# Kernel tuning notes

Hardware: AMD Instinct MI355X
Metric: run time of the kernel (lower is better)

Reference implementation:

```python
import jax, jax.numpy as jnp
import numpy as np

KERNEL = (3, 3, 3)
STRIDE = (1, 1, 1)
PAD = (1, 1, 1)
DIL = (1, 1, 1)


def _deform_unfold_3d(x, offset):
    # x: [B, C, D, H, W]; offset: [B, 3*K, Do, Ho, Wo] with per-tap (dd, dh, dw) order.
    B, C, D, H, W = x.shape
    kd, kh, kw = KERNEL
    K = kd * kh * kw
    Do = (D + 2 * PAD[0] - (DIL[0] * (kd - 1) + 1)) // STRIDE[0] + 1
    Ho = (H + 2 * PAD[1] - (DIL[1] * (kh - 1) + 1)) // STRIDE[1] + 1
    Wo = (W + 2 * PAD[2] - (DIL[2] * (kw - 1) + 1)) // STRIDE[2] + 1
    P = Do * Ho * Wo
    dt = x.dtype
    # kernel-tap base displacements, flattened to [K]
    ki, kj, kk = jnp.meshgrid(jnp.arange(kd), jnp.arange(kh), jnp.arange(kw), indexing="ij")
    bd = (ki.reshape(-1) * DIL[0] - PAD[0]).astype(dt)
    bh = (kj.reshape(-1) * DIL[1] - PAD[1]).astype(dt)
    bw = (kk.reshape(-1) * DIL[2] - PAD[2]).astype(dt)
    # output-grid anchor positions, flattened to [P]
    od, oh, ow = jnp.meshgrid(jnp.arange(Do), jnp.arange(Ho), jnp.arange(Wo), indexing="ij")
    gd = (od.reshape(-1) * STRIDE[0]).astype(dt)
    gh = (oh.reshape(-1) * STRIDE[1]).astype(dt)
    gw = (ow.reshape(-1) * STRIDE[2]).astype(dt)
    off = offset.reshape(B, K, 3, P)
    # sampling positions [B, K, P]
    pd = bd[None, :, None] + gd[None, None, :] + off[:, :, 0]
    ph = bh[None, :, None] + gh[None, None, :] + off[:, :, 1]
    pw = bw[None, :, None] + gw[None, None, :] + off[:, :, 2]
    d0f = jnp.floor(pd); fd = pd - d0f; d0 = d0f.astype(jnp.int32)
    h0f = jnp.floor(ph); fh = ph - h0f; h0 = h0f.astype(jnp.int32)
    w0f = jnp.floor(pw); fw = pw - w0f; w0 = w0f.astype(jnp.int32)
    xflat = x.reshape(B, C, D * H * W)
    out = jnp.zeros((B, C, K, P), dt)
    for ci in (0, 1):
        dsel = d0 + ci
        wd = (1.0 - fd) if ci == 0 else fd
        for cj in (0, 1):
            hsel = h0 + cj
            wh = (1.0 - fh) if cj == 0 else fh
            for ck in (0, 1):
                wsel = w0 + ck
                ww = (1.0 - fw) if ck == 0 else fw
                valid = (dsel >= 0) & (dsel < D) & (hsel >= 0) & (hsel < H) & (wsel >= 0) & (wsel < W)
                idx = (jnp.clip(dsel, 0, D - 1) * H + jnp.clip(hsel, 0, H - 1)) * W + jnp.clip(wsel, 0, W - 1)
                wgt = jnp.where(valid, wd * wh * ww, jnp.zeros((), dt))  # [B, K, P]
                val = jnp.take_along_axis(xflat, idx.reshape(B, 1, K * P), axis=2).reshape(B, C, K, P)
                out = out + wgt[:, None] * val
    return out.reshape(B, C * K, P)  # im2col columns, channel-major then kernel tap


def setup_inputs() -> dict:
    key = jax.random.key(0)
    k1, k2 = jax.random.split(key)
    inp = jax.random.normal(k1, (2, 16, 24, 48, 48), dtype=jnp.float32)
    offset = jax.random.normal(k2, (2, 81, 24, 48, 48), dtype=jnp.float32)
    return {"input": inp, "offset": offset}


def reference(input, offset):
    return _deform_unfold_3d(input, offset)
```

## Files before the change

### kernel.cpp

```cpp
#include <hip/hip_runtime.h>
#include <hip/hip_bf16.h>

typedef float f4 __attribute__((ext_vector_type(4)));
typedef unsigned int u32;
typedef u32 u4 __attribute__((ext_vector_type(4)));

constexpr int B = 2, C = 16, D = 24, H = 48, W = 48;
constexpr int K = 27;
constexpr int SP = D * H * W;
constexpr int HW = H * W;

__device__ inline ushort bf16_bits(float f) {
    __hip_bfloat16 h = __float2bfloat16(f);
    return __builtin_bit_cast(ushort, h);
}

__global__ __launch_bounds__(256) void xpose_bf16_kernel(const float* __restrict__ x,
                                                         u32* __restrict__ xt) {
    int t = blockIdx.x * blockDim.x + threadIdx.x;
    if (t >= B * SP) return;
    int s = t % SP, b = t / SP;
    const float* src = x + (size_t)b * C * SP + s;
    u4 pk[2];
#pragma unroll
    for (int m = 0; m < 8; ++m) {
        float lo = src[(size_t)(2 * m) * SP];
        float hi = src[(size_t)(2 * m + 1) * SP];
        pk[m >> 2][m & 3] = (u32)bf16_bits(lo) | ((u32)bf16_bits(hi) << 16);
    }
    u4* dst = reinterpret_cast<u4*>(xt + (size_t)t * 8);
    dst[0] = pk[0];
    dst[1] = pk[1];
}

__global__ __launch_bounds__(256, 8) void deform_bf16_kernel(const u32* __restrict__ xt,
                                                             const float* __restrict__ off,
                                                             float* __restrict__ out) {
    const int tid = blockIdx.x * blockDim.x + threadIdx.x;
    const int q = tid & 1;
    const int u = tid >> 1;
    const int p = u % SP;
    const int bk = u / SP;
    const int k = bk % K, b = bk / K;

    const float* ob = off + ((size_t)b * (3 * K) + 3 * k) * SP + p;
    float offd = __builtin_nontemporal_load(ob);
    float offh = __builtin_nontemporal_load(ob + (size_t)SP);
    float offw = __builtin_nontemporal_load(ob + (size_t)2 * SP);

    int od = p / HW, rem = p - od * HW;
    int oh = rem / W, ow = rem - oh * W;
    int ki = k / 9, kr = k - ki * 9;
    int kj = kr / 3, kk = kr - kj * 3;

    float pd = (float)(od + ki - 1) + offd;
    float ph = (float)(oh + kj - 1) + offh;
    float pw = (float)(ow + kk - 1) + offw;

    float d0f = floorf(pd), h0f = floorf(ph), w0f = floorf(pw);
    float fd = pd - d0f, fh = ph - h0f, fw = pw - w0f;
    int d0 = (int)d0f, h0 = (int)h0f, w0 = (int)w0f;

    const u4* xb = reinterpret_cast<const u4*>(xt) + (size_t)b * SP * 2 + q;

    float acc[8] = {};
#pragma unroll
    for (int ci = 0; ci < 2; ++ci) {
        int ds = d0 + ci;
        bool vd = (ds >= 0) & (ds < D);
        float wd = ci ? fd : 1.0f - fd;
        int dc = min(max(ds, 0), D - 1);
#pragma unroll
        for (int cj = 0; cj < 2; ++cj) {
            int hs = h0 + cj;
            bool vh = (hs >= 0) & (hs < H);
            float wh = cj ? fh : 1.0f - fh;
            int hc = min(max(hs, 0), H - 1);
#pragma unroll
            for (int ck = 0; ck < 2; ++ck) {
                int ws = w0 + ck;
                bool vw = (ws >= 0) & (ws < W);
                float ww = ck ? fw : 1.0f - fw;
                int wc = min(max(ws, 0), W - 1);
                float wgt = (vd & vh & vw) ? wd * wh * ww : 0.0f;
                int idx = (dc * H + hc) * W + wc;
                u4 v = xb[(size_t)idx * 2];
#pragma unroll
                for (int m = 0; m < 4; ++m) {
                    u32 wbits = v[m];
                    float lo = __builtin_bit_cast(float, wbits << 16);
                    float hi = __builtin_bit_cast(float, wbits & 0xffff0000u);
                    acc[2 * m] += wgt * lo;
                    acc[2 * m + 1] += wgt * hi;
                }
            }
        }
    }

    __shared__ float lds[4][16][36];
    const int l = threadIdx.x & 63;
    const int wv = threadIdx.x >> 6;
    const int c = l >> 1;
    float(*tile)[36] = lds[wv];
#pragma unroll
    for (int j = 0; j < 8; ++j) tile[8 * q + j][c] = acc[j];
    __syncthreads();

    const size_t p_base = (size_t)(p - c);
    float* obase = out + (((size_t)b * C) * K + k) * SP + p_base;
#pragma unroll
    for (int r = 0; r < 2; ++r) {
        int ch = 8 * r + (l >> 3);
        int p0 = 4 * (l & 7);
        f4 v = *reinterpret_cast<const f4*>(&tile[ch][p0]);
        *reinterpret_cast<f4*>(obase + (size_t)ch * K * SP + p0) = v;
    }
}

__global__ __launch_bounds__(256) void deform_kernel_nat(const float* __restrict__ x,
                                                         const float* __restrict__ off,
                                                         float* __restrict__ out) {
    int tid = blockIdx.x * blockDim.x + threadIdx.x;
    if (tid >= B * K * SP) return;
    int p = tid % SP;
    int bk = tid / SP;
    int k = bk % K, b = bk / K;

    const float* ob = off + ((size_t)b * (3 * K) + 3 * k) * SP + p;
    float offd = ob[0];
    float offh = ob[(size_t)SP];
    float offw = ob[(size_t)2 * SP];

    int od = p / HW, rem = p - od * HW;
    int oh = rem / W, ow = rem - oh * W;
    int ki = k / 9, kr = k - ki * 9;
    int kj = kr / 3, kk = kr - kj * 3;

    float pd = (float)(od + ki - 1) + offd;
    float ph = (float)(oh + kj - 1) + offh;
    float pw = (float)(ow + kk - 1) + offw;

    float d0f = floorf(pd), h0f = floorf(ph), w0f = floorf(pw);
    float fd = pd - d0f, fh = ph - h0f, fw = pw - w0f;
    int d0 = (int)d0f, h0 = (int)h0f, w0 = (int)w0f;

    f4 acc[4] = {};
#pragma unroll
    for (int ci = 0; ci < 2; ++ci) {
        int ds = d0 + ci;
        bool vd = (ds >= 0) & (ds < D);
        float wd = ci ? fd : 1.0f - fd;
        int dc = min(max(ds, 0), D - 1);
#pragma unroll
        for (int cj = 0; cj < 2; ++cj) {
            int hs = h0 + cj;
            bool vh = (hs >= 0) & (hs < H);
            float wh = cj ? fh : 1.0f - fh;
            int hc = min(max(hs, 0), H - 1);
#pragma unroll
            for (int ck = 0; ck < 2; ++ck) {
                int ws = w0 + ck;
                bool vw = (ws >= 0) & (ws < W);
                float ww = ck ? fw : 1.0f - fw;
                int wc = min(max(ws, 0), W - 1);
                float wgt = (vd & vh & vw) ? wd * wh * ww : 0.0f;
                int idx = (dc * H + hc) * W + wc;
                const float* src = x + (size_t)b * C * SP + idx;
#pragma unroll
                for (int c2 = 0; c2 < C; ++c2)
                    acc[c2 >> 2][c2 & 3] += wgt * src[(size_t)c2 * SP];
            }
        }
    }

    float* o = out + ((size_t)b * C * K + k) * SP + p;
#pragma unroll
    for (int c2 = 0; c2 < C; ++c2)
        o[(size_t)c2 * K * SP] = acc[c2 >> 2][c2 & 3];
}

extern "C" void kernel_launch(void* const* d_in, const int* in_sizes, int n_in,
                              void* d_out, int out_size, void* d_ws, size_t ws_size,
                              hipStream_t stream) {
    const float* x = (const float*)d_in[0];
    const float* off = (const float*)d_in[1];
    float* out = (float*)d_out;

    const size_t xt_bytes = (size_t)B * SP * 16 * sizeof(ushort);

    if (ws_size >= xt_bytes) {
        u32* xt = (u32*)d_ws;
        const int n_x = B * SP;
        xpose_bf16_kernel<<<(n_x + 255) / 256, 256, 0, stream>>>(x, xt);
        const long long n2 = (long long)B * K * SP * 2;
        const int grid2 = (int)((n2 + 255) / 256);
        deform_bf16_kernel<<<grid2, 256, 0, stream>>>(xt, off, out);
    } else {
        const int n_main = B * K * SP;
        deform_kernel_nat<<<(n_main + 255) / 256, 256, 0, stream>>>(x, off, out);
    }
}
```

Before: 116.3 us.

## Loop each thread over half the kernel taps with double-buffered LDS tiles

The deformable gather kernel now gives each thread a fixed (batch, position, channel-half) and has it loop over 13 or 14 kernel taps, instead of launching one thread per tap. The LDS transpose tile is double-buffered by tap parity, so each iteration needs one barrier before the coalesced output store. This cuts per-thread index setup and launch size, and may improve locality of gathers across neighbouring taps. In exchange the grid shrinks by roughly a factor of 13, which lowers occupancy and leaves less parallelism to hide gather latency.

```diff
diff --git a/kernel.cpp b/kernel.cpp
--- a/kernel.cpp
+++ b/kernel.cpp
@@ -33,87 +33,96 @@
     dst[1] = pk[1];
 }
 
-__global__ __launch_bounds__(256, 8) void deform_bf16_kernel(const u32* __restrict__ xt,
-                                                             const float* __restrict__ off,
-                                                             float* __restrict__ out) {
+__global__ __launch_bounds__(256, 8) void deform_bf16_k(const u32* __restrict__ xt,
+                                                        const float* __restrict__ off,
+                                                        float* __restrict__ out) {
     const int tid = blockIdx.x * blockDim.x + threadIdx.x;
     const int q = tid & 1;
-    const int u = tid >> 1;
-    const int p = u % SP;
-    const int bk = u / SP;
-    const int k = bk % K, b = bk / K;
-
-    const float* ob = off + ((size_t)b * (3 * K) + 3 * k) * SP + p;
-    float offd = __builtin_nontemporal_load(ob);
-    float offh = __builtin_nontemporal_load(ob + (size_t)SP);
-    float offw = __builtin_nontemporal_load(ob + (size_t)2 * SP);
-
-    int od = p / HW, rem = p - od * HW;
-    int oh = rem / W, ow = rem - oh * W;
-    int ki = k / 9, kr = k - ki * 9;
-    int kj = kr / 3, kk = kr - kj * 3;
-
-    float pd = (float)(od + ki - 1) + offd;
-    float ph = (float)(oh + kj - 1) + offh;
-    float pw = (float)(ow + kk - 1) + offw;
-
-    float d0f = floorf(pd), h0f = floorf(ph), w0f = floorf(pw);
-    float fd = pd - d0f, fh = ph - h0f, fw = pw - w0f;
-    int d0 = (int)d0f, h0 = (int)h0f, w0 = (int)w0f;
-
+    const int t = tid >> 1;
+    const int p = t % SP;
+    const int r = t / SP;
+    const int khalf = r & 1;
+    const int b = r >> 1;
+
+    const int od = p / HW;
+    const int rem = p - od * HW;
+    const int oh = rem / W, ow = rem - oh * W;
+
+    const float* obp = off + (size_t)b * (3 * K) * SP + p;
     const u4* xb = reinterpret_cast<const u4*>(xt) + (size_t)b * SP * 2 + q;
 
-    float acc[8] = {};
-#pragma unroll
-    for (int ci = 0; ci < 2; ++ci) {
-        int ds = d0 + ci;
-        bool vd = (ds >= 0) & (ds < D);
-        float wd = ci ? fd : 1.0f - fd;
-        int dc = min(max(ds, 0), D - 1);
-#pragma unroll
-        for (int cj = 0; cj < 2; ++cj) {
-            int hs = h0 + cj;
-            bool vh = (hs >= 0) & (hs < H);
-            float wh = cj ? fh : 1.0f - fh;
-            int hc = min(max(hs, 0), H - 1);
-#pragma unroll
-            for (int ck = 0; ck < 2; ++ck) {
-                int ws = w0 + ck;
-                bool vw = (ws >= 0) & (ws < W);
-                float ww = ck ? fw : 1.0f - fw;
-                int wc = min(max(ws, 0), W - 1);
-                float wgt = (vd & vh & vw) ? wd * wh * ww : 0.0f;
-                int idx = (dc * H + hc) * W + wc;
-                u4 v = xb[(size_t)idx * 2];
-#pragma unroll
-                for (int m = 0; m < 4; ++m) {
-                    u32 wbits = v[m];
-                    float lo = __builtin_bit_cast(float, wbits << 16);
-                    float hi = __builtin_bit_cast(float, wbits & 0xffff0000u);
-                    acc[2 * m] += wgt * lo;
-                    acc[2 * m + 1] += wgt * hi;
+    __shared__ float lds[2][4][16][36];
+    const int l = threadIdx.x & 63;
+    const int wv = threadIdx.x >> 6;
+    const int c = l >> 1;
+    const size_t p_base = (size_t)(p - c);
+    const int ch_lo = l >> 3;
+    const int p0 = 4 * (l & 7);
+    float* osb = out + ((size_t)b * C * K) * SP + p_base + p0;
+
+    const int k_beg = khalf ? 14 : 0;
+    const int k_end = khalf ? 27 : 14;
+#pragma unroll 2
+    for (int k = k_beg; k < k_end; ++k) {
+        const int ki = k / 9, kr2 = k - ki * 9;
+        const int kj = kr2 / 3, kk = kr2 - kj * 3;
+
+        float offd = __builtin_nontemporal_load(obp + (size_t)(3 * k) * SP);
+        float offh = __builtin_nontemporal_load(obp + (size_t)(3 * k + 1) * SP);
+        float offw = __builtin_nontemporal_load(obp + (size_t)(3 * k + 2) * SP);
+
+        float pd = (float)(od + ki - 1) + offd;
+        float ph = (float)(oh + kj - 1) + offh;
+        float pw = (float)(ow + kk - 1) + offw;
+
+        float d0f = floorf(pd), h0f = floorf(ph), w0f = floorf(pw);
+        float fd = pd - d0f, fh = ph - h0f, fw = pw - w0f;
+        int d0 = (int)d0f, h0 = (int)h0f, w0 = (int)w0f;
+
+        float acc[8] = {};
+#pragma unroll
+        for (int ci = 0; ci < 2; ++ci) {
+            int ds = d0 + ci;
+            bool vd = (ds >= 0) & (ds < D);
+            float wd = ci ? fd : 1.0f - fd;
+            int dc = min(max(ds, 0), D - 1);
+#pragma unroll
+            for (int cj = 0; cj < 2; ++cj) {
+                int hs = h0 + cj;
+                bool vh = (hs >= 0) & (hs < H);
+                float wh = cj ? fh : 1.0f - fh;
+                int hc = min(max(hs, 0), H - 1);
+#pragma unroll
+                for (int ck = 0; ck < 2; ++ck) {
+                    int ws = w0 + ck;
+                    bool vw = (ws >= 0) & (ws < W);
+                    float ww = ck ? fw : 1.0f - fw;
+                    int wc = min(max(ws, 0), W - 1);
+                    float wgt = (vd & vh & vw) ? wd * wh * ww : 0.0f;
+                    int idx = (dc * H + hc) * W + wc;
+                    u4 v = xb[(size_t)idx * 2];
+#pragma unroll
+                    for (int m = 0; m < 4; ++m) {
+                        u32 wbits = v[m];
+                        float lo = __builtin_bit_cast(float, wbits << 16);
+                        float hi = __builtin_bit_cast(float, wbits & 0xffff0000u);
+                        acc[2 * m] += wgt * lo;
+                        acc[2 * m + 1] += wgt * hi;
+                    }
                 }
             }
         }
-    }
-
-    __shared__ float lds[4][16][36];
-    const int l = threadIdx.x & 63;
-    const int wv = threadIdx.x >> 6;
-    const int c = l >> 1;
-    float(*tile)[36] = lds[wv];
-#pragma unroll
-    for (int j = 0; j < 8; ++j) tile[8 * q + j][c] = acc[j];
-    __syncthreads();
-
-    const size_t p_base = (size_t)(p - c);
-    float* obase = out + (((size_t)b * C) * K + k) * SP + p_base;
-#pragma unroll
-    for (int r = 0; r < 2; ++r) {
-        int ch = 8 * r + (l >> 3);
-        int p0 = 4 * (l & 7);
-        f4 v = *reinterpret_cast<const f4*>(&tile[ch][p0]);
-        *reinterpret_cast<f4*>(obase + (size_t)ch * K * SP + p0) = v;
+
+        float(*tile)[36] = lds[k & 1][wv];
+#pragma unroll
+        for (int j = 0; j < 8; ++j) tile[8 * q + j][c] = acc[j];
+        __syncthreads();
+#pragma unroll
+        for (int rr = 0; rr < 2; ++rr) {
+            int ch = 8 * rr + ch_lo;
+            f4 vv = *reinterpret_cast<const f4*>(&tile[ch][p0]);
+            *reinterpret_cast<f4*>(osb + ((size_t)ch * K + k) * SP) = vv;
+        }
     }
 }
 
@@ -192,9 +201,9 @@
         u32* xt = (u32*)d_ws;
         const int n_x = B * SP;
         xpose_bf16_kernel<<<(n_x + 255) / 256, 256, 0, stream>>>(x, xt);
-        const long long n2 = (long long)B * K * SP * 2;
-        const int grid2 = (int)((n2 + 255) / 256);
-        deform_bf16_kernel<<<grid2, 256, 0, stream>>>(xt, off, out);
+        const long long n_thr = (long long)B * SP * 2 * 2;
+        const int grid = (int)(n_thr / 256);
+        deform_bf16_k<<<grid, 256, 0, stream>>>(xt, off, out);
     } else {
         const int n_main = B * K * SP;
         deform_kernel_nat<<<(n_main + 255) / 256, 256, 0, stream>>>(x, off, out);
```

Result: slower. 146.5 us (+26.0%).

## Compute all 16 channels per thread instead of splitting across thread pairs

Applied to the files above, without the earlier changes.

Each thread now handles one (b,k,p) sample with all 16 channels, loading both 16-byte bf16 records per corner, instead of two threads splitting 8 channels each. This halves the thread count and removes the duplicated offset loads, index math and bilinear weight computation per sample. The LDS transpose tile grows to 64 positions per wave and stores go out as 256-byte contiguous rows per channel. Per-thread register use rises, and the launch bound drops to 4 blocks per CU, which may reduce occupancy and memory-latency hiding for the gathers.

```diff
diff --git a/kernel.cpp b/kernel.cpp
--- a/kernel.cpp
+++ b/kernel.cpp
@@ -33,26 +33,25 @@
     dst[1] = pk[1];
 }
 
-__global__ __launch_bounds__(256, 8) void deform_bf16_kernel(const u32* __restrict__ xt,
-                                                             const float* __restrict__ off,
-                                                             float* __restrict__ out) {
+__global__ __launch_bounds__(256, 4) void deform_bf16_c16(const u32* __restrict__ xt,
+                                                          const float* __restrict__ off,
+                                                          float* __restrict__ out) {
     const int tid = blockIdx.x * blockDim.x + threadIdx.x;
-    const int q = tid & 1;
-    const int u = tid >> 1;
-    const int p = u % SP;
-    const int bk = u / SP;
+    const int p = tid % SP;
+    const int bk = tid / SP;
     const int k = bk % K, b = bk / K;
+
+    const int od = p / HW;
+    const int rem = p - od * HW;
+    const int oh = rem / W, ow = rem - oh * W;
+    const int ki = k / 9, kr2 = k - ki * 9;
+    const int kj = kr2 / 3, kk = kr2 - kj * 3;
 
     const float* ob = off + ((size_t)b * (3 * K) + 3 * k) * SP + p;
     float offd = __builtin_nontemporal_load(ob);
     float offh = __builtin_nontemporal_load(ob + (size_t)SP);
     float offw = __builtin_nontemporal_load(ob + (size_t)2 * SP);
 
-    int od = p / HW, rem = p - od * HW;
-    int oh = rem / W, ow = rem - oh * W;
-    int ki = k / 9, kr = k - ki * 9;
-    int kj = kr / 3, kk = kr - kj * 3;
-
     float pd = (float)(od + ki - 1) + offd;
     float ph = (float)(oh + kj - 1) + offh;
     float pw = (float)(ow + kk - 1) + offw;
@@ -61,9 +60,9 @@
     float fd = pd - d0f, fh = ph - h0f, fw = pw - w0f;
     int d0 = (int)d0f, h0 = (int)h0f, w0 = (int)w0f;
 
-    const u4* xb = reinterpret_cast<const u4*>(xt) + (size_t)b * SP * 2 + q;
-
-    float acc[8] = {};
+    const u4* xb = reinterpret_cast<const u4*>(xt) + (size_t)b * SP * 2;
+
+    float acc[16] = {};
 #pragma unroll
     for (int ci = 0; ci < 2; ++ci) {
         int ds = d0 + ci;
@@ -84,36 +83,40 @@
                 int wc = min(max(ws, 0), W - 1);
                 float wgt = (vd & vh & vw) ? wd * wh * ww : 0.0f;
                 int idx = (dc * H + hc) * W + wc;
-                u4 v = xb[(size_t)idx * 2];
+                const u4* rec = xb + (size_t)idx * 2;
+                u4 v0 = rec[0];
+                u4 v1 = rec[1];
 #pragma unroll
                 for (int m = 0; m < 4; ++m) {
-                    u32 wbits = v[m];
-                    float lo = __builtin_bit_cast(float, wbits << 16);
-                    float hi = __builtin_bit_cast(float, wbits & 0xffff0000u);
-                    acc[2 * m] += wgt * lo;
-                    acc[2 * m + 1] += wgt * hi;
+                    u32 wb = v0[m];
+                    acc[2 * m]     += wgt * __builtin_bit_cast(float, wb << 16);
+                    acc[2 * m + 1] += wgt * __builtin_bit_cast(float, wb & 0xffff0000u);
+                }
+#pragma unroll
+                for (int m = 0; m < 4; ++m) {
+                    u32 wb = v1[m];
+                    acc[8 + 2 * m] += wgt * __builtin_bit_cast(float, wb << 16);
+                    acc[9 + 2 * m] += wgt * __builtin_bit_cast(float, wb & 0xffff0000u);
                 }
             }
         }
     }
 
-    __shared__ float lds[4][16][36];
+    __shared__ float tile[4][16][68];
     const int l = threadIdx.x & 63;
     const int wv = threadIdx.x >> 6;
-    const int c = l >> 1;
-    float(*tile)[36] = lds[wv];
-#pragma unroll
-    for (int j = 0; j < 8; ++j) tile[8 * q + j][c] = acc[j];
+#pragma unroll
+    for (int j = 0; j < 16; ++j) tile[wv][j][l] = acc[j];
     __syncthreads();
 
-    const size_t p_base = (size_t)(p - c);
-    float* obase = out + (((size_t)b * C) * K + k) * SP + p_base;
-#pragma unroll
-    for (int r = 0; r < 2; ++r) {
-        int ch = 8 * r + (l >> 3);
-        int p0 = 4 * (l & 7);
-        f4 v = *reinterpret_cast<const f4*>(&tile[ch][p0]);
-        *reinterpret_cast<f4*>(obase + (size_t)ch * K * SP + p0) = v;
+    const int p_base = p - l;
+    const int colbase = 4 * (l & 15);
+    const int choff = l >> 4;
+#pragma unroll
+    for (int pass = 0; pass < 4; ++pass) {
+        int ch = pass * 4 + choff;
+        f4 vv = *reinterpret_cast<const f4*>(&tile[wv][ch][colbase]);
+        *reinterpret_cast<f4*>(out + (((size_t)b * C + ch) * K + k) * SP + p_base + colbase) = vv;
     }
 }
 
@@ -192,9 +195,9 @@
         u32* xt = (u32*)d_ws;
         const int n_x = B * SP;
         xpose_bf16_kernel<<<(n_x + 255) / 256, 256, 0, stream>>>(x, xt);
-        const long long n2 = (long long)B * K * SP * 2;
-        const int grid2 = (int)((n2 + 255) / 256);
-        deform_bf16_kernel<<<grid2, 256, 0, stream>>>(xt, off, out);
+        const int n_main = B * K * SP;
+        const int grid = n_main / 256;
+        deform_bf16_c16<<<grid, 256, 0, stream>>>(xt, off, out);
     } else {
         const int n_main = B * K * SP;
         deform_kernel_nat<<<(n_main + 255) / 256, 256, 0, stream>>>(x, off, out);
```

Result: slower. 135.9 us (+16.9%).
